# Optimization experiments

Measured on AMD Instinct MI355X. Metric: run time of the kernel, lower is better.

The kernel has to match this reference:

```python
import jax, jax.numpy as jnp
import numpy as np

H_DIM = 64
GRID = 8
NS = 2.0  # neighborhood_size
S = 256   # number of sequences (scenes)
P = 64    # pedestrians per sequence
EPS = 1e-5


def setup_inputs() -> dict:
    key = jax.random.key(0)
    k = jax.random.split(key, 6)
    N = S * P
    G = GRID * GRID
    h_states = jax.random.normal(k[0], (1, N, H_DIM), jnp.float32)
    end_pos = jax.random.normal(k[1], (N, 2), jnp.float32)
    starts = (jnp.arange(S, dtype=jnp.int32) * P)
    seq_start_end = jnp.stack([starts, starts + P], axis=1)  # (S, 2)
    # mlp_pool: Linear(G*H_DIM -> H_DIM) + BatchNorm1d + ReLU
    W = jax.random.normal(k[2], (G * H_DIM, H_DIM), jnp.float32) / np.sqrt(G * H_DIM)
    b = jnp.zeros((H_DIM,), jnp.float32)
    gamma = jnp.ones((H_DIM,), jnp.float32)
    beta = jnp.zeros((H_DIM,), jnp.float32)
    return {"h_states": h_states, "seq_start_end": seq_start_end, "end_pos": end_pos,
            "W": W, "b": b, "gamma": gamma, "beta": beta}


def reference(h_states, seq_start_end, end_pos, W, b, gamma, beta):
    nseq = seq_start_end.shape[0]          # S (static)
    N = end_pos.shape[0]
    Hd = h_states.shape[-1]
    nped = N // nseq                       # P (static; equal-length sequences)
    G = GRID * GRID
    half = NS / 2.0

    h = h_states.reshape(N, Hd).reshape(nseq, nped, Hd)     # (S, P, H)
    pos = end_pos.reshape(nseq, nped, 2)                    # (S, P, 2)

    # bounds per center pedestrian i
    tl_x = pos[..., 0] - half   # (S, P)
    tl_y = pos[..., 1] + half
    br_x = pos[..., 0] + half
    br_y = pos[..., 1] - half

    # pairwise: axis 1 = center i, axis 2 = other k
    ox = pos[:, None, :, 0]     # (S, 1, P)
    oy = pos[:, None, :, 1]
    cell_x = jnp.floor((ox - tl_x[:, :, None]) / NS * GRID)
    cell_y = jnp.floor((tl_y[:, :, None] - oy) / NS * GRID)
    grid = cell_x + cell_y * GRID                            # (S, P, P)

    oob = ((ox >= br_x[:, :, None]) | (ox <= tl_x[:, :, None]) |
           (oy >= tl_y[:, :, None]) | (oy <= br_y[:, :, None]))
    diag = jnp.eye(nped, dtype=bool)[None]                   # self excluded (within_bound[0::P+1]=1)
    valid = (~oob) & (~diag)

    grid_i = jnp.clip(grid.astype(jnp.int32), 0, G - 1)      # masked entries don't matter
    seq_off = (jnp.arange(nseq, dtype=jnp.int32)[:, None, None] * nped
               + jnp.arange(nped, dtype=jnp.int32)[None, :, None]) * G
    dummy = nseq * nped * G
    ids = jnp.where(valid, seq_off + grid_i, dummy)          # (S, P, P)

    # data for (s, i, k) is hidden of other k (curr_hidden.repeat(num_ped, 1))
    data = jnp.broadcast_to(h[:, None, :, :], (nseq, nped, nped, Hd)).reshape(-1, Hd)
    pooled = jax.ops.segment_sum(data, ids.reshape(-1), num_segments=dummy + 1)[:-1]
    x = pooled.reshape(N, G * Hd)                            # (N, G*H), row i = concat over grid cells

    # mlp_pool: Linear -> BatchNorm1d (train mode, biased var) -> ReLU
    x = x @ W + b
    mu = jnp.mean(x, axis=0)
    var = jnp.mean((x - mu) ** 2, axis=0)
    x = gamma * (x - mu) / jnp.sqrt(var + EPS) + beta
    return jnp.maximum(x, 0.0)
```

## Files before the change

### kernel.cpp

```cpp
#include <hip/hip_runtime.h>
#include <hip/hip_bf16.h>


#define NSEQ 256
#define NTOT (NSEQ*64)
#define EPSV 1e-5f

typedef __attribute__((ext_vector_type(8))) short short8;
typedef __attribute__((ext_vector_type(4))) float f32x4;
typedef unsigned short ushort_t;

__device__ __forceinline__ ushort_t f2b(float f) {
    __hip_bfloat16 h = __float2bfloat16(f);
    return *reinterpret_cast<ushort_t*>(&h);
}
__device__ __forceinline__ int kperm(int k) {
    return ((k >> 5)*2 + ((k & 7) >> 2))*16 + ((k >> 3) & 3)*4 + (k & 3);
}

__global__ __launch_bounds__(256) void sp_transpose(
    const float* __restrict__ W, short* __restrict__ Wt, float* __restrict__ statbuf)
{
    __shared__ __align__(16) float Tl[64*68];
    const int b = blockIdx.x, tid = threadIdx.x;
    if (b == 0) {
        #pragma unroll
        for (int q = 0; q < 8; ++q) statbuf[q*256 + tid] = 0.0f;
    }
    const float* wg = W + (size_t)b*4096;
    for (int m = 0; m < 4; ++m) {
        int c = m*256 + tid;
        int k = c >> 4, t0 = (c & 15)*4;
        *(f32x4*)(Tl + k*68 + t0) = *(const f32x4*)(wg + k*64 + t0);
    }
    __syncthreads();
    for (int m = 0; m < 2; ++m) {
        int q = m*256 + tid;
        int col = q >> 3, k0 = (q & 7)*8;
        short8 o;
        #pragma unroll
        for (int i2 = 0; i2 < 8; ++i2)
            o[i2] = (short)f2b(Tl[kperm(k0 + i2)*68 + col]);
        *(short8*)(Wt + ((size_t)(b*64 + col)*64 + k0)) = o;
    }
}

#define SM_CM    9216
#define SM_POS   13312
#define SM_HF    13824
#define SM_XSA1  8704
#define SM_XSB0  17408
#define SM_XSB1  26112
#define SM_REDA  34816
#define SM_REDB  36864
#define SM_TOT   38912

__global__ __launch_bounds__(1024, 2) void sp_main(
    const float* __restrict__ h, const float* __restrict__ pos,
    const short* __restrict__ Wt, const float* __restrict__ bvec,
    float* __restrict__ X, float* __restrict__ statbuf)
{
    __shared__ __align__(16) char smem[SM_TOT];
    ushort_t*      Ht = (ushort_t*)(smem);
    unsigned char* cm = (unsigned char*)(smem + SM_CM);
    float*         px = (float*)(smem + SM_POS);
    float*         py = px + 64;
    short*         Hf = (short*)(smem + SM_HF);

    const int b    = blockIdx.x;
    const int base = b * 64;
    const int tid  = threadIdx.x;
    const int lane = tid & 63, w = tid >> 6;
    const int wl   = w & 7;
    const int half = w >> 3;
    const int row0 = half * 32;
    const int ln15 = lane & 15, ln4 = lane >> 4;
    const int xph  = (b >> 3) & 7;

    if (tid < 64) { px[tid] = pos[(base + tid)*2]; py[tid] = pos[(base + tid)*2 + 1]; }
    {
        int j = tid >> 4, t0 = (tid & 15)*4;
        f32x4 v = *(const f32x4*)(h + (size_t)(base + j)*64 + t0);
        #pragma unroll
        for (int u = 0; u < 4; ++u) Ht[(t0 + u)*72 + j] = f2b(v[u]);
    }
    __syncthreads();

    for (int m = 0; m < 4; ++m) {
        int p = m*1024 + tid;
        int i = p >> 6, j = p & 63;
        unsigned char val = 255;
        if (i != j) {
            float ax = px[i], ay = py[i], ox = px[j], oy = py[j];
            float tlx = ax - 1.0f, tly = ay + 1.0f, brx = ax + 1.0f, bry = ay - 1.0f;
            bool oob = (ox >= brx) | (ox <= tlx) | (oy >= tly) | (oy <= bry);
            if (!oob) {
                int g = (int)(floorf((ox - tlx)*4.0f) + floorf((tly - oy)*4.0f)*8.0f);
                g = g < 0 ? 0 : (g > 63 ? 63 : g);
                val = (unsigned char)g;
            }
        }
        cm[i*64 + j] = val;
    }
    if (tid < 64) {
        #pragma unroll
        for (int f = 0; f < 8; ++f) {
            int mt = f >> 1, kt2 = f & 1;
            short8 v = *(const short8*)(Ht + (mt*16 + ln15)*72 + kt2*32 + ln4*8);
            *(short8*)(Hf + (f*64 + lane)*8) = v;
        }
    }
    __syncthreads();

    unsigned ohw[2][2][2];
    {
        const unsigned w8 = (unsigned)(wl * 8);
        #pragma unroll
        for (int rt = 0; rt < 2; ++rt)
            #pragma unroll
            for (int kt = 0; kt < 2; ++kt) {
                const unsigned* cp = (const unsigned*)(cm + (row0 + rt*16 + ln15)*64 + kt*32 + ln4*8);
                #pragma unroll
                for (int hf2 = 0; hf2 < 2; ++hf2) {
                    unsigned cw = cp[hf2], oh = 0u;
                    #pragma unroll
                    for (int u = 0; u < 4; ++u) {
                        unsigned d = ((cw >> (8*u)) & 255u) - w8;
                        if (d < 8u) oh |= (1u << d) << (8*u);
                    }
                    ohw[rt][kt][hf2] = oh;
                }
            }
    }

    f32x4 acc[2][4];
    #pragma unroll
    for (int rt = 0; rt < 2; ++rt)
        #pragma unroll
        for (int nt = 0; nt < 4; ++nt) acc[rt][nt] = (f32x4){0.f,0.f,0.f,0.f};

    for (int cc = 0; cc < 8; ++cc) {
        const int c2 = (cc + xph) & 7;
        const int g  = wl*8 + c2;
        const short* wgp = Wt + (size_t)g*4096;
        short8 bw[2][4];
        #pragma unroll
        for (int kt = 0; kt < 2; ++kt)
            #pragma unroll
            for (int nt = 0; nt < 4; ++nt)
                bw[kt][nt] = *(const short8*)(wgp + (nt*16 + ln15)*64 + kt*32 + ln4*8);

        #pragma unroll
        for (int rt = 0; rt < 2; ++rt) {
            short8 sf[2];
            #pragma unroll
            for (int kt = 0; kt < 2; ++kt) {
                unsigned t0 = (ohw[rt][kt][0] >> c2) & 0x01010101u;
                unsigned t1 = (ohw[rt][kt][1] >> c2) & 0x01010101u;
                union { unsigned u[4]; short8 s; } sfu;
                sfu.u[0] = ((t0 & 1u)          | ((t0 << 8) & 0x10000u)) * 0x3F80u;
                sfu.u[1] = (((t0 >> 16) & 1u)  | ((t0 >> 8) & 0x10000u)) * 0x3F80u;
                sfu.u[2] = ((t1 & 1u)          | ((t1 << 8) & 0x10000u)) * 0x3F80u;
                sfu.u[3] = (((t1 >> 16) & 1u)  | ((t1 >> 8) & 0x10000u)) * 0x3F80u;
                sf[kt] = sfu.s;
            }
            f32x4 pt[4];
            #pragma unroll
            for (int mt = 0; mt < 4; ++mt) pt[mt] = (f32x4){0.f,0.f,0.f,0.f};
            #pragma unroll
            for (int kt2 = 0; kt2 < 2; ++kt2) {
                short8 hm[4];
                #pragma unroll
                for (int mt = 0; mt < 4; ++mt)
                    hm[mt] = *(const short8*)(Hf + (((mt*2 + kt2)*64 + lane))*8);
                #pragma unroll
                for (int mt = 0; mt < 4; ++mt)
                    pt[mt] = __builtin_amdgcn_mfma_f32_16x16x32_bf16(hm[mt], sf[kt2], pt[mt], 0, 0, 0);
            }
            #pragma unroll
            for (int kt = 0; kt < 2; ++kt) {
                short8 af;
                #pragma unroll
                for (int r = 0; r < 4; ++r) {
                    af[r]     = (short)f2b(pt[2*kt    ][r]);
                    af[4 + r] = (short)f2b(pt[2*kt + 1][r]);
                }
                #pragma unroll
                for (int nt = 0; nt < 4; ++nt)
                    acc[rt][nt] = __builtin_amdgcn_mfma_f32_16x16x32_bf16(af, bw[kt][nt], acc[rt][nt], 0, 0, 0);
            }
        }
    }
    __syncthreads();

    float* XsA0 = (float*)smem;
    float* XsA1 = (float*)(smem + SM_XSA1);
    float* XsB0 = (float*)(smem + SM_XSB0);
    float* XsB1 = (float*)(smem + SM_XSB1);
    for (int step = 0; step < 4; ++step) {
        if ((wl & 3) == step) {
            float* Xs = half ? ((wl < 4) ? XsB0 : XsB1)
                             : ((wl < 4) ? XsA0 : XsA1);
            #pragma unroll
            for (int rt = 0; rt < 2; ++rt)
                #pragma unroll
                for (int nt = 0; nt < 4; ++nt)
                    #pragma unroll
                    for (int r = 0; r < 4; ++r) {
                        int row = rt*16 + ln4*4 + r;
                        int col = nt*16 + ln15;
                        if (step == 0) Xs[row*68 + col]  = acc[rt][nt][r];
                        else           Xs[row*68 + col] += acc[rt][nt][r];
                    }
        }
        __syncthreads();
    }

    {
        const int hh = tid >> 9, t = tid & 511;
        const int lr = t >> 4, c0 = (t & 15)*4;
        const float* Y0 = hh ? XsB0 : XsA0;
        const float* Y1 = hh ? XsB1 : XsA1;
        float* xg = X + (size_t)(base + hh*32 + lr)*64 + c0;
        f32x4 v;
        #pragma unroll
        for (int u = 0; u < 4; ++u) {
            int o = lr*68 + c0 + u;
            v[u] = Y0[o] + Y1[o] + bvec[c0 + u];
        }
        *(f32x4*)xg = v;
    }

    {
        float* redA1 = (float*)(smem + SM_REDA);
        float* redA2 = redA1 + 256;
        float* redB1 = (float*)(smem + SM_REDB);
        float* redB2 = redB1 + 256;
        if (tid < 256 || (tid >= 512 && tid < 768)) {
            int hh = tid >> 9, t = tid & 255;
            int col = t & 63, rg = t >> 6;
            const float* Y0 = hh ? XsB0 : XsA0;
            const float* Y1 = hh ? XsB1 : XsA1;
            float* r1 = hh ? redB1 : redA1;
            float* r2 = hh ? redB2 : redA2;
            float bc = bvec[col], s1 = 0.f, s2 = 0.f;
            for (int ii = 0; ii < 8; ++ii) {
                int o = (rg*8 + ii)*68 + col;
                float xv = Y0[o] + Y1[o] + bc;
                s1 += xv; s2 += xv*xv;
            }
            r1[rg*64 + col] = s1;
            r2[rg*64 + col] = s2;
        }
        __syncthreads();
        if (tid < 128 || (tid >= 512 && tid < 640)) {
            int hh = tid >> 9, t = tid & 127;
            int hs = t >> 6, c2 = t & 63;
            const float* r0 = hh ? (hs ? redB2 : redB1) : (hs ? redA2 : redA1);
            float v = r0[c2] + r0[64 + c2] + r0[128 + c2] + r0[192 + c2];
            atomicAdd(statbuf + (b & 15)*128 + hs*64 + c2, v);
        }
    }
}

__global__ __launch_bounds__(256) void sp_finish(
    float* __restrict__ X, const float* __restrict__ statbuf,
    const float* __restrict__ gamma, const float* __restrict__ beta)
{
    __shared__ float scale[64], shift[64];
    const int b = blockIdx.x, tid = threadIdx.x;

    if (tid < 64) {
        const float inv_n = 1.0f / (float)NTOT;
        float s1 = 0.f, s2 = 0.f;
        #pragma unroll
        for (int s = 0; s < 16; ++s) {
            s1 += statbuf[s*128 + tid];
            s2 += statbuf[s*128 + 64 + tid];
        }
        float mu  = s1 * inv_n;
        float var = s2 * inv_n - mu*mu;
        float sc  = gamma[tid] / sqrtf(var + EPSV);
        scale[tid] = sc;
        shift[tid] = beta[tid] - mu*sc;
    }
    __syncthreads();
    #pragma unroll
    for (int q = 0; q < 4; ++q) {
        size_t idx4 = (size_t)b*1024 + q*256 + tid;
        f32x4 v = ((f32x4*)X)[idx4];
        int c0 = ((int)idx4*4) & 63;
        #pragma unroll
        for (int u = 0; u < 4; ++u)
            v[u] = fmaxf(v[u]*scale[c0 + u] + shift[c0 + u], 0.0f);
        ((f32x4*)X)[idx4] = v;
    }
}

extern "C" void kernel_launch(void* const* d_in, const int* in_sizes, int n_in,
                              void* d_out, int out_size, void* d_ws, size_t ws_size,
                              hipStream_t stream)
{
    const float* h     = (const float*)d_in[0];
    const float* pos   = (const float*)d_in[2];
    const float* W     = (const float*)d_in[3];
    const float* bvec  = (const float*)d_in[4];
    const float* gamma = (const float*)d_in[5];
    const float* beta  = (const float*)d_in[6];

    float* X       = (float*)d_out;
    short* Wt      = (short*)d_ws;
    float* statbuf = (float*)((char*)d_ws + 524288);

    sp_transpose<<<64,   256,  0, stream>>>(W, Wt, statbuf);
    sp_main     <<<NSEQ, 1024, 0, stream>>>(h, pos, Wt, bvec, X, statbuf);
    sp_finish   <<<NSEQ, 256,  0, stream>>>(X, statbuf, gamma, beta);
}
```

Measured before the change: 110.0 us.

## Fuse BatchNorm finish into main kernel via grid-wide atomic barrier

Removes the separate sp_finish launch by having every block of sp_main wait on a global atomic counter once all column statistics are accumulated. Each block then computes the scale and shift and applies BN plus ReLU to its tile while it is still in shared memory, writing X only once. This drops one kernel launch and a full read-modify-write pass over the output. In exchange it relies on all 256 blocks being co-resident; with 1024-thread blocks at two per CU this should hold on a large GPU, otherwise the barrier would deadlock.

```diff
diff --git a/kernel.cpp b/kernel.cpp
--- a/kernel.cpp
+++ b/kernel.cpp
@@ -19,13 +19,15 @@
 }
 
 __global__ __launch_bounds__(256) void sp_transpose(
-    const float* __restrict__ W, short* __restrict__ Wt, float* __restrict__ statbuf)
+    const float* __restrict__ W, short* __restrict__ Wt, float* __restrict__ statbuf,
+    unsigned* __restrict__ ctr)
 {
     __shared__ __align__(16) float Tl[64*68];
     const int b = blockIdx.x, tid = threadIdx.x;
     if (b == 0) {
         #pragma unroll
         for (int q = 0; q < 8; ++q) statbuf[q*256 + tid] = 0.0f;
+        if (tid == 0) *ctr = 0u;
     }
     const float* wg = W + (size_t)b*4096;
     for (int m = 0; m < 4; ++m) {
@@ -58,7 +60,8 @@
 __global__ __launch_bounds__(1024, 2) void sp_main(
     const float* __restrict__ h, const float* __restrict__ pos,
     const short* __restrict__ Wt, const float* __restrict__ bvec,
-    float* __restrict__ X, float* __restrict__ statbuf)
+    const float* __restrict__ gamma, const float* __restrict__ beta,
+    float* __restrict__ X, float* __restrict__ statbuf, unsigned* __restrict__ ctr)
 {
     __shared__ __align__(16) char smem[SM_TOT];
     ushort_t*      Ht = (ushort_t*)(smem);
@@ -214,21 +217,6 @@
                     }
         }
         __syncthreads();
-    }
-
-    {
-        const int hh = tid >> 9, t = tid & 511;
-        const int lr = t >> 4, c0 = (t & 15)*4;
-        const float* Y0 = hh ? XsB0 : XsA0;
-        const float* Y1 = hh ? XsB1 : XsA1;
-        float* xg = X + (size_t)(base + hh*32 + lr)*64 + c0;
-        f32x4 v;
-        #pragma unroll
-        for (int u = 0; u < 4; ++u) {
-            int o = lr*68 + c0 + u;
-            v[u] = Y0[o] + Y1[o] + bvec[c0 + u];
-        }
-        *(f32x4*)xg = v;
     }
 
     {
@@ -261,22 +249,27 @@
             atomicAdd(statbuf + (b & 15)*128 + hs*64 + c2, v);
         }
     }
-}
-
-__global__ __launch_bounds__(256) void sp_finish(
-    float* __restrict__ X, const float* __restrict__ statbuf,
-    const float* __restrict__ gamma, const float* __restrict__ beta)
-{
-    __shared__ float scale[64], shift[64];
-    const int b = blockIdx.x, tid = threadIdx.x;
-
+
+    __syncthreads();
+    if (tid == 0) {
+        __hip_atomic_fetch_add(ctr, 1u, __ATOMIC_RELEASE, __HIP_MEMORY_SCOPE_AGENT);
+        unsigned v;
+        do {
+            v = __hip_atomic_load(ctr, __ATOMIC_ACQUIRE, __HIP_MEMORY_SCOPE_AGENT);
+            if (v < (unsigned)NSEQ) __builtin_amdgcn_s_sleep(8);
+        } while (v < (unsigned)NSEQ);
+    }
+    __syncthreads();
+
+    float* scale = (float*)(smem + SM_REDA);
+    float* shift = scale + 64;
     if (tid < 64) {
         const float inv_n = 1.0f / (float)NTOT;
         float s1 = 0.f, s2 = 0.f;
         #pragma unroll
         for (int s = 0; s < 16; ++s) {
-            s1 += statbuf[s*128 + tid];
-            s2 += statbuf[s*128 + 64 + tid];
+            s1 += __hip_atomic_load(statbuf + s*128 + tid,      __ATOMIC_RELAXED, __HIP_MEMORY_SCOPE_AGENT);
+            s2 += __hip_atomic_load(statbuf + s*128 + 64 + tid, __ATOMIC_RELAXED, __HIP_MEMORY_SCOPE_AGENT);
         }
         float mu  = s1 * inv_n;
         float var = s2 * inv_n - mu*mu;
@@ -285,15 +278,20 @@
         shift[tid] = beta[tid] - mu*sc;
     }
     __syncthreads();
-    #pragma unroll
-    for (int q = 0; q < 4; ++q) {
-        size_t idx4 = (size_t)b*1024 + q*256 + tid;
-        f32x4 v = ((f32x4*)X)[idx4];
-        int c0 = ((int)idx4*4) & 63;
-        #pragma unroll
-        for (int u = 0; u < 4; ++u)
-            v[u] = fmaxf(v[u]*scale[c0 + u] + shift[c0 + u], 0.0f);
-        ((f32x4*)X)[idx4] = v;
+    {
+        const int hh = tid >> 9, t = tid & 511;
+        const int lr = t >> 4, c0 = (t & 15)*4;
+        const float* Y0 = hh ? XsB0 : XsA0;
+        const float* Y1 = hh ? XsB1 : XsA1;
+        float* xg = X + (size_t)(base + hh*32 + lr)*64 + c0;
+        f32x4 v;
+        #pragma unroll
+        for (int u = 0; u < 4; ++u) {
+            int o = lr*68 + c0 + u;
+            float xv = Y0[o] + Y1[o] + bvec[c0 + u];
+            v[u] = fmaxf(xv*scale[c0 + u] + shift[c0 + u], 0.0f);
+        }
+        *(f32x4*)xg = v;
     }
 }
 
@@ -308,11 +306,11 @@
     const float* gamma = (const float*)d_in[5];
     const float* beta  = (const float*)d_in[6];
 
-    float* X       = (float*)d_out;
-    short* Wt      = (short*)d_ws;
-    float* statbuf = (float*)((char*)d_ws + 524288);
-
-    sp_transpose<<<64,   256,  0, stream>>>(W, Wt, statbuf);
-    sp_main     <<<NSEQ, 1024, 0, stream>>>(h, pos, Wt, bvec, X, statbuf);
-    sp_finish   <<<NSEQ, 256,  0, stream>>>(X, statbuf, gamma, beta);
-}
+    float* X        = (float*)d_out;
+    short* Wt       = (short*)d_ws;
+    float* statbuf  = (float*)((char*)d_ws + 524288);
+    unsigned* ctr   = (unsigned*)((char*)d_ws + 532480);
+
+    sp_transpose<<<64,   256,  0, stream>>>(W, Wt, statbuf, ctr);
+    sp_main     <<<NSEQ, 1024, 0, stream>>>(h, pos, Wt, bvec, gamma, beta, X, statbuf, ctr);
+}
```

Result: slower. 122.0 us (+10.9%).
